# Optimization experiments

Hardware: AMD Instinct MI355X
Metric: run time of the kernel (lower is better)

## Reference

```python
import jax, jax.numpy as jnp
import numpy as np

B, T, E, D, A, H, C, K = 32, 1500, 512, 512, 512, 4, 10, 201
SHARPENING = 1.0


def setup_inputs() -> dict:
    key = jax.random.key(0)
    ks = jax.random.split(key, 11)
    def w(k, shape, fan_in):
        return jax.random.normal(k, shape, jnp.float32) / np.sqrt(fan_in).astype(np.float32)
    return {
        "enc_out": jax.random.normal(ks[0], (B, T, E), jnp.float32),
        "x_lens": jax.random.randint(ks[1], (B,), T // 2, T + 1),
        "dec_out": jax.random.normal(ks[2], (B, 1, D), jnp.float32),
        # previous-step attention weights: a valid distribution over T per head
        "aw_step": jax.nn.softmax(jax.random.normal(ks[3], (B, T, H), jnp.float32), axis=1),
        "w_enc": w(ks[4], (H, E, A), E),   # per-head LinearND(enc->att)
        "b_enc": jnp.zeros((H, A), jnp.float32),
        "w_dec": w(ks[5], (H, D, A), D),   # per-head LinearND(dec->att), no bias
        "w_conv": w(ks[6], (H, C, A), C),  # per-head LinearND(conv_ch->att), no bias
        "conv_k": w(ks[7], (H * C, 1, K), K),  # grouped 1D conv kernels (O,I,K), groups=H
        "v": w(ks[8], (H, A), A),          # per-head LinearND(att->1), no bias
        "w_mha": w(ks[9], (H * E, E), H * E),
        "b_mha": jnp.zeros((E,), jnp.float32),
    }


def reference(enc_out, x_lens, dec_out, aw_step, w_enc, b_enc, w_dec, w_conv, conv_k, v, w_mha, b_mha):
    b, t, e = enc_out.shape
    h = aw_step.shape[-1]
    c = w_conv.shape[1]
    k = conv_k.shape[-1]
    # enc_out_a: per-head encoder projection [B,T,H,A]
    enc_a = jnp.einsum('bte,hea->btha', enc_out, w_enc) + b_enc
    # decoder projection, broadcast over time [B,1,H,A]
    dec_a = jnp.einsum('bd,hda->bha', dec_out[:, 0], w_dec)[:, None]
    # location features: grouped 1D conv over previous attention weights
    aw_t = jnp.transpose(aw_step, (0, 2, 1))  # [B,H,T]
    conv = jax.lax.conv_general_dilated(
        aw_t, conv_k, window_strides=(1,), padding=[(k // 2, k // 2)],
        dimension_numbers=('NCH', 'OIH', 'NCH'), feature_group_count=h)  # [B,H*C,T]
    conv = conv.reshape(b, h, c, t).transpose(0, 3, 1, 2)  # [B,T,H,C]
    conv_a = jnp.einsum('bthc,hca->btha', conv, w_conv)
    # additive energy [B,T,H]
    energy = jnp.einsum('btha,ha->bth', jnp.tanh(enc_a + dec_a + conv_a), v)
    # original code multiplies energy by mask (1 valid, -1024 padded) then sharpening
    mask = jnp.where(jnp.arange(t)[None, :] < x_lens[:, None], 1.0, -1024.0).astype(energy.dtype)
    energy = energy * mask[:, :, None] * SHARPENING
    aw = jax.nn.softmax(energy, axis=1)  # softmax over time per head
    # per-head context, concatenated along feature dim -> [B,1,H*E]
    ctx = jnp.einsum('bte,bth->bhe', enc_out, aw).reshape(b, 1, h * e)
    ctx = ctx @ w_mha + b_mha  # [B,1,E]
    return ctx, aw
```

## Files before the change

### kernel.cpp

```cpp
#include <hip/hip_runtime.h>
#include <hip/hip_bf16.h>

#define BB 32
#define TT 1500
#define TP 1536
#define EE 512
#define HH 4
#define AA 512
#define NN 2048
#define CC 10
#define KCONV 201
#define KAUG 576

typedef __attribute__((ext_vector_type(8))) __bf16 bf16x8;
typedef __attribute__((ext_vector_type(4))) float f32x4;

__device__ __forceinline__ unsigned short f2bf(float x) {
    unsigned int u = __float_as_uint(x);
    u = (u + 0x7fffu + ((u >> 16) & 1u)) >> 16;
    return (unsigned short)u;
}
__device__ __forceinline__ float bf2f(unsigned short u) {
    return __uint_as_float(((unsigned int)u) << 16);
}
__device__ __forceinline__ void glds16(const void* g, void* l) {
    __builtin_amdgcn_global_load_lds(
        (const __attribute__((address_space(1))) unsigned int*)g,
        (__attribute__((address_space(3))) unsigned int*)l, 16, 0, 0);
}
__device__ __forceinline__ float tanh_fast(float x) {
    float e = __expf(x * 2.0f);
    return fmaf(-2.0f, __builtin_amdgcn_rcpf(e + 1.0f), 1.0f);
}

#define PREP_DEC0   0
#define PREP_CONV0  1024
#define PREP_WT0    8704
#define PREP_PAD0   13312
#define PREP_ENC0   20404
#define PREP_TOTAL  44404

__global__ __launch_bounds__(256) void k_prep(
    const float* __restrict__ enc, const int* __restrict__ xl,
    const float* __restrict__ dec_out, const float* __restrict__ aw_step,
    const float* __restrict__ w_enc, const float* __restrict__ b_enc,
    const float* __restrict__ w_dec, const float* __restrict__ w_conv,
    const float* __restrict__ conv_k,
    unsigned short* __restrict__ Whi, unsigned short* __restrict__ Wlo,
    unsigned short* __restrict__ Ahi, unsigned short* __restrict__ Alo,
    float* __restrict__ dec_a) {
    __shared__ float sbuf[456 + KCONV];
    const int bid = blockIdx.x;
    const int tid = threadIdx.x;

    if (bid < PREP_CONV0) {
        const int b  = bid >> 5;
        const int n0 = (bid & 31) * 64;
        const int n  = n0 + (tid & 63);
        const int dg = tid >> 6;
        const int h  = n >> 9, a = n & 511;
        const float* dp = dec_out + (size_t)b * 512 + dg * 128;
        const float* wp = w_dec + ((size_t)h * 512 + dg * 128) * 512 + a;
        float acc = 0.f;
#pragma unroll 8
        for (int d = 0; d < 128; ++d) acc += dp[d] * wp[(size_t)d * 512];
        sbuf[tid] = acc;
        __syncthreads();
        if (tid < 64) {
            float tot = sbuf[tid] + sbuf[tid + 64] + sbuf[tid + 128] + sbuf[tid + 192];
            dec_a[(size_t)b * NN + n0 + tid] = b_enc[n0 + tid] + tot;
        }
    } else if (bid < PREP_WT0) {
        int r = bid - PREP_CONV0;
        const int tch = r % 6;
        const int hc  = (r / 6) % 40;
        const int b   = r / 240;
        const int h   = hc / 10;
        const int t0  = tch * 256;
        float* sAw = sbuf;
        float* sK  = sbuf + 456;
        for (int i = tid; i < 456; i += 256) {
            int ts = t0 - 100 + i;
            sAw[i] = (ts >= 0 && ts < TT) ? aw_step[((size_t)b * TT + ts) * HH + h] : 0.f;
        }
        if (tid < KCONV) sK[tid] = conv_k[(size_t)hc * KCONV + tid];
        __syncthreads();
        int t = t0 + tid;
        if (t < TT) {
            float acc = 0.f;
            for (int k = 0; k < KCONV; ++k) acc += sAw[tid + k] * sK[k];
            size_t o = ((size_t)b * TP + t) * KAUG + 512 + hc;
            unsigned short hi = f2bf(acc);
            Ahi[o] = hi; Alo[o] = f2bf(acc - bf2f(hi));
        }
    } else if (bid < PREP_PAD0) {
        int idx = (bid - PREP_WT0) * 256 + tid;
        int n = idx / KAUG, k = idx % KAUG;
        int h = n >> 9, a = n & 511;
        float val = 0.f;
        if (k < 512) {
            val = w_enc[((size_t)h * 512 + k) * 512 + a];
        } else if (k < 552) {
            int j = k - 512; int h2 = j / 10, c = j % 10;
            if (h2 == h) val = w_conv[((size_t)h * 10 + c) * 512 + a];
        }
        unsigned short hi = f2bf(val);
        Whi[idx] = hi;
        Wlo[idx] = f2bf(val - bf2f(hi));
    } else if (bid < PREP_ENC0) {
        int idx = (bid - PREP_PAD0) * 256 + tid;
        const int tot1 = BB * 36 * KAUG;
        const int tot2 = BB * TT * 24;
        size_t o;
        if (idx < tot1) {
            int b = idx / (36 * KAUG); int r2 = idx % (36 * KAUG);
            int t = 1500 + r2 / KAUG;  int k = r2 % KAUG;
            o = ((size_t)b * TP + t) * KAUG + k;
        } else if (idx < tot1 + tot2) {
            int j = idx - tot1;
            int b = j / (TT * 24); int r2 = j % (TT * 24);
            int t = r2 / 24;       int k = 552 + r2 % 24;
            o = ((size_t)b * TP + t) * KAUG + k;
        } else return;
        Ahi[o] = 0; Alo[o] = 0;
    } else {
        long idx = (long)(bid - PREP_ENC0) * 256 + tid;
        if (idx >= 6144000L) return;
        long f = idx * 4;
        int b = (int)(f / 768000);
        int r2 = (int)(f % 768000);
        int t = r2 >> 9, e = r2 & 511;
        float4 vv = *reinterpret_cast<const float4*>(enc + f);
        ushort4 h4;
        h4.x = f2bf(vv.x); h4.y = f2bf(vv.y); h4.z = f2bf(vv.z); h4.w = f2bf(vv.w);
        size_t o = ((size_t)b * TP + t) * KAUG + e;
        *reinterpret_cast<ushort4*>(Ahi + o) = h4;
        if (((t & ~127) + 128) > xl[b]) {
            ushort4 l4;
            l4.x = f2bf(vv.x - bf2f(h4.x));
            l4.y = f2bf(vv.y - bf2f(h4.y));
            l4.z = f2bf(vv.z - bf2f(h4.z));
            l4.w = f2bf(vv.w - bf2f(h4.w));
            *reinterpret_cast<ushort4*>(Alo + o) = l4;
        }
    }
}

__global__ __launch_bounds__(256) void k_gemm(
    const unsigned short* __restrict__ Ahi, const unsigned short* __restrict__ Alo,
    const unsigned short* __restrict__ Whi, const unsigned short* __restrict__ Wlo,
    const float* __restrict__ dec_a, const float* __restrict__ vvec,
    const int* __restrict__ xl, float* __restrict__ energy) {
    __shared__ unsigned short lsAhi[128 * 32], lsAlo[128 * 32];
    __shared__ unsigned short lsBhi[128 * 32], lsBlo[128 * 32];
    const int ntile = blockIdx.x, mtile = blockIdx.y, b = blockIdx.z;
    const int tid = threadIdx.x;
    const int lane = tid & 63, wave = tid >> 6;
    const int wm = wave >> 1, wn = wave & 1;
    const int m0 = mtile * 128, n0 = ntile * 128;
    const int xlen = xl[b];

    f32x4 acc[4][4];
#pragma unroll
    for (int i = 0; i < 4; i++)
#pragma unroll
        for (int j = 0; j < 4; j++) acc[i][j] = (f32x4){0.f, 0.f, 0.f, 0.f};

    const int row = tid >> 2;
    const int ko  = (tid & 3) * 8;
    const size_t abase = ((size_t)b * TP + m0 + row) * KAUG + ko;
    const size_t bbase = ((size_t)n0 + row) * KAUG + ko;
    const int l1 = row * 32 + ko;
    const int l2 = l1 + 64 * 32;
    const int ar = wm * 64, br = wn * 64;
    const int fo = (lane & 15) * 32 + (lane >> 4) * 8;

    if (m0 + 128 > xlen) {
        for (int ks = 0; ks < 18; ++ks) {
            const int k0 = ks * 32;
            __syncthreads();
            glds16(Ahi + abase + k0,                     &lsAhi[l1]);
            glds16(Ahi + abase + k0 + (size_t)64 * KAUG, &lsAhi[l2]);
            glds16(Alo + abase + k0,                     &lsAlo[l1]);
            glds16(Alo + abase + k0 + (size_t)64 * KAUG, &lsAlo[l2]);
            glds16(Whi + bbase + k0,                     &lsBhi[l1]);
            glds16(Whi + bbase + k0 + (size_t)64 * KAUG, &lsBhi[l2]);
            glds16(Wlo + bbase + k0,                     &lsBlo[l1]);
            glds16(Wlo + bbase + k0 + (size_t)64 * KAUG, &lsBlo[l2]);
            asm volatile("s_waitcnt vmcnt(0)" ::: "memory");
            __syncthreads();

            bf16x8 ah[4], al[4], bh[4], bl[4];
#pragma unroll
            for (int i = 0; i < 4; i++) {
                ah[i] = *(const bf16x8*)&lsAhi[(ar + i * 16) * 32 + fo];
                al[i] = *(const bf16x8*)&lsAlo[(ar + i * 16) * 32 + fo];
                bh[i] = *(const bf16x8*)&lsBhi[(br + i * 16) * 32 + fo];
                bl[i] = *(const bf16x8*)&lsBlo[(br + i * 16) * 32 + fo];
            }
#pragma unroll
            for (int i = 0; i < 4; i++)
#pragma unroll
                for (int j = 0; j < 4; j++) {
                    acc[i][j] = __builtin_amdgcn_mfma_f32_16x16x32_bf16(ah[i], bh[j], acc[i][j], 0, 0, 0);
                    acc[i][j] = __builtin_amdgcn_mfma_f32_16x16x32_bf16(ah[i], bl[j], acc[i][j], 0, 0, 0);
                    acc[i][j] = __builtin_amdgcn_mfma_f32_16x16x32_bf16(al[i], bh[j], acc[i][j], 0, 0, 0);
                }
        }
    } else {
        for (int ks = 0; ks < 18; ++ks) {
            const int k0 = ks * 32;
            __syncthreads();
            glds16(Ahi + abase + k0,                     &lsAhi[l1]);
            glds16(Ahi + abase + k0 + (size_t)64 * KAUG, &lsAhi[l2]);
            glds16(Whi + bbase + k0,                     &lsBhi[l1]);
            glds16(Whi + bbase + k0 + (size_t)64 * KAUG, &lsBhi[l2]);
            asm volatile("s_waitcnt vmcnt(0)" ::: "memory");
            __syncthreads();

            bf16x8 ah[4], bh[4];
#pragma unroll
            for (int i = 0; i < 4; i++) {
                ah[i] = *(const bf16x8*)&lsAhi[(ar + i * 16) * 32 + fo];
                bh[i] = *(const bf16x8*)&lsBhi[(br + i * 16) * 32 + fo];
            }
#pragma unroll
            for (int i = 0; i < 4; i++)
#pragma unroll
                for (int j = 0; j < 4; j++)
                    acc[i][j] = __builtin_amdgcn_mfma_f32_16x16x32_bf16(ah[i], bh[j], acc[i][j], 0, 0, 0);
        }
    }

    const int h = ntile >> 2;
    const int kg = lane >> 4;
    float dv[4], vv[4];
#pragma unroll
    for (int j = 0; j < 4; j++) {
        int ng = n0 + wn * 64 + j * 16 + (lane & 15);
        dv[j] = dec_a[(size_t)b * NN + ng];
        vv[j] = vvec[ng];
    }
#pragma unroll
    for (int i = 0; i < 4; i++) {
        float part[4] = {0.f, 0.f, 0.f, 0.f};
#pragma unroll
        for (int j = 0; j < 4; j++)
#pragma unroll
            for (int r = 0; r < 4; r++)
                part[r] += tanh_fast(acc[i][j][r] + dv[j]) * vv[j];
#pragma unroll
        for (int r = 0; r < 4; r++) {
            float s = part[r];
            s += __shfl_xor(s, 1, 64);
            s += __shfl_xor(s, 2, 64);
            s += __shfl_xor(s, 4, 64);
            s += __shfl_xor(s, 8, 64);
            if ((lane & 15) == 0) {
                int t = m0 + wm * 64 + i * 16 + kg * 4 + r;
                if (t < TT)
                    atomicAdd(&energy[((size_t)b * HH + h) * TP + t], s);
            }
        }
    }
}

__global__ __launch_bounds__(512) void k_softmax(const float* __restrict__ energy,
                                                 const int* __restrict__ x_lens,
                                                 float* __restrict__ aw) {
    const int b = blockIdx.x >> 2, h = blockIdx.x & 3;
    const int tid = threadIdx.x;
    __shared__ float sE[TT];
    __shared__ float red[512];
    const int xlen = x_lens[b];
    float lmax = -3.4e38f;
    for (int t = tid; t < TT; t += 512) {
        float e = energy[((size_t)b * HH + h) * TP + t];
        float m = (t < xlen) ? e : e * -1024.0f;
        sE[t] = m;
        lmax = fmaxf(lmax, m);
    }
    red[tid] = lmax; __syncthreads();
    for (int s = 256; s > 0; s >>= 1) { if (tid < s) red[tid] = fmaxf(red[tid], red[tid + s]); __syncthreads(); }
    float mx = red[0]; __syncthreads();
    float lsum = 0.f;
    for (int t = tid; t < TT; t += 512) {
        float ex = expf(sE[t] - mx);
        sE[t] = ex; lsum += ex;
    }
    red[tid] = lsum; __syncthreads();
    for (int s = 256; s > 0; s >>= 1) { if (tid < s) red[tid] += red[tid + s]; __syncthreads(); }
    float sum = red[0];
    for (int t = tid; t < TT; t += 512)
        aw[((size_t)b * TT + t) * HH + h] = sE[t] / sum;
}

__global__ __launch_bounds__(512) void k_ctx(const float* __restrict__ enc,
                                             const float* __restrict__ aw,
                                             float* __restrict__ ctx_h) {
    const int chunk = blockIdx.x, b = blockIdx.y;
    const int t0 = chunk * 128;
    const int nt = (TT - t0 < 128) ? (TT - t0) : 128;
    __shared__ float sA[128 * 4];
    const int tid = threadIdx.x;
    for (int i = tid; i < nt * 4; i += 512)
        sA[i] = aw[((size_t)b * TT + t0) * HH + i];
    __syncthreads();
    float a0 = 0.f, a1 = 0.f, a2 = 0.f, a3 = 0.f;
    const float* ep = enc + ((size_t)b * TT + t0) * EE + tid;
    if (nt == 128) {
#pragma unroll 8
        for (int tt = 0; tt < 128; ++tt) {
            float ev = ep[(size_t)tt * EE];
            a0 += sA[tt * 4 + 0] * ev; a1 += sA[tt * 4 + 1] * ev;
            a2 += sA[tt * 4 + 2] * ev; a3 += sA[tt * 4 + 3] * ev;
        }
    } else {
        for (int tt = 0; tt < nt; ++tt) {
            float ev = ep[(size_t)tt * EE];
            a0 += sA[tt * 4 + 0] * ev; a1 += sA[tt * 4 + 1] * ev;
            a2 += sA[tt * 4 + 2] * ev; a3 += sA[tt * 4 + 3] * ev;
        }
    }
    atomicAdd(&ctx_h[((size_t)b * HH + 0) * EE + tid], a0);
    atomicAdd(&ctx_h[((size_t)b * HH + 1) * EE + tid], a1);
    atomicAdd(&ctx_h[((size_t)b * HH + 2) * EE + tid], a2);
    atomicAdd(&ctx_h[((size_t)b * HH + 3) * EE + tid], a3);
}

__global__ __launch_bounds__(256) void k_mha(const float* __restrict__ ctx_h,
                                             const float* __restrict__ w_mha,
                                             const float* __restrict__ b_mha,
                                             float* __restrict__ out) {
    __shared__ float sred[256];
    const int tid = threadIdx.x;
    const int b  = blockIdx.x >> 2;
    const int eo = ((blockIdx.x & 3) << 7) + (tid & 127);
    const int kg = tid >> 7;
    const float* c = ctx_h + (size_t)b * NN + kg * 1024;
    const float* w = w_mha + ((size_t)kg * 1024) * EE + eo;
    float acc = 0.f;
#pragma unroll 8
    for (int k = 0; k < 1024; ++k) acc += c[k] * w[(size_t)k * EE];
    sred[tid] = acc;
    __syncthreads();
    if (tid < 128)
        out[(size_t)b * EE + eo] = b_mha[eo] + sred[tid] + sred[tid + 128];
}

extern "C" void kernel_launch(void* const* d_in, const int* in_sizes, int n_in,
                              void* d_out, int out_size, void* d_ws, size_t ws_size,
                              hipStream_t stream) {
    (void)in_sizes; (void)n_in; (void)out_size;
    const float* enc    = (const float*)d_in[0];
    const int*   xlen   = (const int*)d_in[1];
    const float* dec    = (const float*)d_in[2];
    const float* aw_in  = (const float*)d_in[3];
    const float* w_enc  = (const float*)d_in[4];
    const float* b_enc  = (const float*)d_in[5];
    const float* w_dec  = (const float*)d_in[6];
    const float* w_conv = (const float*)d_in[7];
    const float* convk  = (const float*)d_in[8];
    const float* v      = (const float*)d_in[9];
    const float* w_mha  = (const float*)d_in[10];
    const float* b_mha  = (const float*)d_in[11];
    float* out = (float*)d_out;

    char* ws = (char*)d_ws;
    unsigned short* Whi = (unsigned short*)ws;
    unsigned short* Wlo = Whi + (size_t)NN * KAUG;
    unsigned short* Ahi = (unsigned short*)(ws + 4718592);
    unsigned short* Alo = Ahi + (size_t)BB * TP * KAUG;
    float* dec_a  = (float*)(ws + 117964800);
    float* energy = (float*)(ws + 118226944);
    float* ctx_h  = (float*)(ws + 119013376);
    (void)ws_size;

    hipMemsetAsync(energy, 0, 786432 + 262144, stream);

    k_prep<<<dim3(PREP_TOTAL), 256, 0, stream>>>(enc, xlen, dec, aw_in, w_enc, b_enc,
                                                 w_dec, w_conv, convk,
                                                 Whi, Wlo, Ahi, Alo, dec_a);
    k_gemm<<<dim3(16, 12, BB), 256, 0, stream>>>(Ahi, Alo, Whi, Wlo, dec_a, v, xlen, energy);
    k_softmax<<<dim3(BB * HH), 512, 0, stream>>>(energy, xlen, out + 16384);
    k_ctx <<<dim3(12, BB), 512, 0, stream>>>(enc, out + 16384, ctx_h);
    k_mha <<<dim3(128), 256, 0, stream>>>(ctx_h, w_mha, b_mha, out);
}
```

Baseline: 597.1 us.

## Fuse fp32-to-bf16 encoder conversion into GEMM for fully valid tiles

After: 603.9 us. About the same (+1.1%).

```diff
diff --git a/kernel.cpp b/kernel.cpp
--- a/kernel.cpp
+++ b/kernel.cpp
@@ -32,13 +32,18 @@
     float e = __expf(x * 2.0f);
     return fmaf(-2.0f, __builtin_amdgcn_rcpf(e + 1.0f), 1.0f);
 }
+__device__ __forceinline__ unsigned int pkbf(float x, float y) {
+    float2 f{x, y};
+    __hip_bfloat162 h2 = __float22bfloat162_rn(f);
+    return *reinterpret_cast<unsigned int*>(&h2);
+}
 
 #define PREP_DEC0   0
 #define PREP_CONV0  1024
 #define PREP_WT0    8704
 #define PREP_PAD0   13312
 #define PREP_ENC0   20404
-#define PREP_TOTAL  44404
+#define PREP_TOTAL  34740
 
 __global__ __launch_bounds__(256) void k_prep(
     const float* __restrict__ enc, const int* __restrict__ xl,
@@ -91,7 +96,8 @@
             for (int k = 0; k < KCONV; ++k) acc += sAw[tid + k] * sK[k];
             size_t o = ((size_t)b * TP + t) * KAUG + 512 + hc;
             unsigned short hi = f2bf(acc);
-            Ahi[o] = hi; Alo[o] = f2bf(acc - bf2f(hi));
+            Ahi[o] = hi;
+            if (((t & ~127) + 128) > xl[b]) Alo[o] = f2bf(acc - bf2f(hi));
         }
     } else if (bid < PREP_PAD0) {
         int idx = (bid - PREP_WT0) * 256 + tid;
@@ -124,41 +130,40 @@
         } else return;
         Ahi[o] = 0; Alo[o] = 0;
     } else {
-        long idx = (long)(bid - PREP_ENC0) * 256 + tid;
-        if (idx >= 6144000L) return;
-        long f = idx * 4;
-        int b = (int)(f / 768000);
-        int r2 = (int)(f % 768000);
-        int t = r2 >> 9, e = r2 & 511;
-        float4 vv = *reinterpret_cast<const float4*>(enc + f);
-        ushort4 h4;
-        h4.x = f2bf(vv.x); h4.y = f2bf(vv.y); h4.z = f2bf(vv.z); h4.w = f2bf(vv.w);
-        size_t o = ((size_t)b * TP + t) * KAUG + e;
+        int r = bid - PREP_ENC0;
+        int b = r / 448;
+        int f4 = (r % 448) * 256 + tid;
+        int rowoff = f4 >> 7;
+        int col = (f4 & 127) * 4;
+        int rstart = xl[b] & ~127;
+        int t = rstart + rowoff;
+        if (t >= TT) return;
+        float4 vv = *reinterpret_cast<const float4*>(enc + ((size_t)b * TT + t) * 512 + col);
+        ushort4 h4, l4;
+        h4.x = f2bf(vv.x); l4.x = f2bf(vv.x - bf2f(h4.x));
+        h4.y = f2bf(vv.y); l4.y = f2bf(vv.y - bf2f(h4.y));
+        h4.z = f2bf(vv.z); l4.z = f2bf(vv.z - bf2f(h4.z));
+        h4.w = f2bf(vv.w); l4.w = f2bf(vv.w - bf2f(h4.w));
+        size_t o = ((size_t)b * TP + t) * KAUG + col;
         *reinterpret_cast<ushort4*>(Ahi + o) = h4;
-        if (((t & ~127) + 128) > xl[b]) {
-            ushort4 l4;
-            l4.x = f2bf(vv.x - bf2f(h4.x));
-            l4.y = f2bf(vv.y - bf2f(h4.y));
-            l4.z = f2bf(vv.z - bf2f(h4.z));
-            l4.w = f2bf(vv.w - bf2f(h4.w));
-            *reinterpret_cast<ushort4*>(Alo + o) = l4;
-        }
-    }
-}
-
-__global__ __launch_bounds__(256) void k_gemm(
-    const unsigned short* __restrict__ Ahi, const unsigned short* __restrict__ Alo,
-    const unsigned short* __restrict__ Whi, const unsigned short* __restrict__ Wlo,
+        *reinterpret_cast<ushort4*>(Alo + o) = l4;
+    }
+}
+
+__global__ __launch_bounds__(256) void k_gemm_v(
+    const float* __restrict__ enc,
+    const unsigned short* __restrict__ Ahi,
+    const unsigned short* __restrict__ Whi,
     const float* __restrict__ dec_a, const float* __restrict__ vvec,
     const int* __restrict__ xl, float* __restrict__ energy) {
-    __shared__ unsigned short lsAhi[128 * 32], lsAlo[128 * 32];
-    __shared__ unsigned short lsBhi[128 * 32], lsBlo[128 * 32];
+    __shared__ unsigned short lsA[128 * 32];
+    __shared__ unsigned short lsB[128 * 32];
     const int ntile = blockIdx.x, mtile = blockIdx.y, b = blockIdx.z;
+    const int m0 = mtile * 128, n0 = ntile * 128;
+    if (m0 + 128 > xl[b]) return;
     const int tid = threadIdx.x;
     const int lane = tid & 63, wave = tid >> 6;
     const int wm = wave >> 1, wn = wave & 1;
-    const int m0 = mtile * 128, n0 = ntile * 128;
-    const int xlen = xl[b];
 
     f32x4 acc[4][4];
 #pragma unroll
@@ -168,68 +173,60 @@
 
     const int row = tid >> 2;
     const int ko  = (tid & 3) * 8;
+    const size_t bbase = ((size_t)n0 + row) * KAUG + ko;
     const size_t abase = ((size_t)b * TP + m0 + row) * KAUG + ko;
-    const size_t bbase = ((size_t)n0 + row) * KAUG + ko;
-    const int l1 = row * 32 + ko;
+    const int l1 = tid * 8;
     const int l2 = l1 + 64 * 32;
+
+    const float* ap0 = enc + ((size_t)b * TT + m0 + row) * 512 + ko;
+    const float* ap1 = ap0 + (size_t)64 * 512;
+
     const int ar = wm * 64, br = wn * 64;
     const int fo = (lane & 15) * 32 + (lane >> 4) * 8;
 
-    if (m0 + 128 > xlen) {
-        for (int ks = 0; ks < 18; ++ks) {
-            const int k0 = ks * 32;
-            __syncthreads();
-            glds16(Ahi + abase + k0,                     &lsAhi[l1]);
-            glds16(Ahi + abase + k0 + (size_t)64 * KAUG, &lsAhi[l2]);
-            glds16(Alo + abase + k0,                     &lsAlo[l1]);
-            glds16(Alo + abase + k0 + (size_t)64 * KAUG, &lsAlo[l2]);
-            glds16(Whi + bbase + k0,                     &lsBhi[l1]);
-            glds16(Whi + bbase + k0 + (size_t)64 * KAUG, &lsBhi[l2]);
-            glds16(Wlo + bbase + k0,                     &lsBlo[l1]);
-            glds16(Wlo + bbase + k0 + (size_t)64 * KAUG, &lsBlo[l2]);
-            asm volatile("s_waitcnt vmcnt(0)" ::: "memory");
-            __syncthreads();
-
-            bf16x8 ah[4], al[4], bh[4], bl[4];
-#pragma unroll
-            for (int i = 0; i < 4; i++) {
-                ah[i] = *(const bf16x8*)&lsAhi[(ar + i * 16) * 32 + fo];
-                al[i] = *(const bf16x8*)&lsAlo[(ar + i * 16) * 32 + fo];
-                bh[i] = *(const bf16x8*)&lsBhi[(br + i * 16) * 32 + fo];
-                bl[i] = *(const bf16x8*)&lsBlo[(br + i * 16) * 32 + fo];
+    float4 fa0 = *(const float4*)(ap0);
+    float4 fa1 = *(const float4*)(ap0 + 4);
+    float4 fa2 = *(const float4*)(ap1);
+    float4 fa3 = *(const float4*)(ap1 + 4);
+
+    for (int ks = 0; ks < 18; ++ks) {
+        const int k0 = ks * 32;
+        __syncthreads();
+        glds16(Whi + bbase + k0,                     &lsB[l1]);
+        glds16(Whi + bbase + k0 + (size_t)64 * KAUG, &lsB[l2]);
+        if (ks < 16) {
+            uint4 w0, w1;
+            w0.x = pkbf(fa0.x, fa0.y); w0.y = pkbf(fa0.z, fa0.w);
+            w0.z = pkbf(fa1.x, fa1.y); w0.w = pkbf(fa1.z, fa1.w);
+            w1.x = pkbf(fa2.x, fa2.y); w1.y = pkbf(fa2.z, fa2.w);
+            w1.z = pkbf(fa3.x, fa3.y); w1.w = pkbf(fa3.z, fa3.w);
+            *reinterpret_cast<uint4*>(&lsA[l1]) = w0;
+            *reinterpret_cast<uint4*>(&lsA[l1 + 2048]) = w1;
+            if (ks < 15) {
+                const int nk = k0 + 32;
+                fa0 = *(const float4*)(ap0 + nk);
+                fa1 = *(const float4*)(ap0 + nk + 4);
+                fa2 = *(const float4*)(ap1 + nk);
+                fa3 = *(const float4*)(ap1 + nk + 4);
             }
-#pragma unroll
-            for (int i = 0; i < 4; i++)
-#pragma unroll
-                for (int j = 0; j < 4; j++) {
-                    acc[i][j] = __builtin_amdgcn_mfma_f32_16x16x32_bf16(ah[i], bh[j], acc[i][j], 0, 0, 0);
-                    acc[i][j] = __builtin_amdgcn_mfma_f32_16x16x32_bf16(ah[i], bl[j], acc[i][j], 0, 0, 0);
-                    acc[i][j] = __builtin_amdgcn_mfma_f32_16x16x32_bf16(al[i], bh[j], acc[i][j], 0, 0, 0);
-                }
-        }
-    } else {
-        for (int ks = 0; ks < 18; ++ks) {
-            const int k0 = ks * 32;
-            __syncthreads();
-            glds16(Ahi + abase + k0,                     &lsAhi[l1]);
-            glds16(Ahi + abase + k0 + (size_t)64 * KAUG, &lsAhi[l2]);
-            glds16(Whi + bbase + k0,                     &lsBhi[l1]);
-            glds16(Whi + bbase + k0 + (size_t)64 * KAUG, &lsBhi[l2]);
-            asm volatile("s_waitcnt vmcnt(0)" ::: "memory");
-            __syncthreads();
-
-            bf16x8 ah[4], bh[4];
-#pragma unroll
-            for (int i = 0; i < 4; i++) {
-                ah[i] = *(const bf16x8*)&lsAhi[(ar + i * 16) * 32 + fo];
-                bh[i] = *(const bf16x8*)&lsBhi[(br + i * 16) * 32 + fo];
-            }
-#pragma unroll
-            for (int i = 0; i < 4; i++)
-#pragma unroll
-                for (int j = 0; j < 4; j++)
-                    acc[i][j] = __builtin_amdgcn_mfma_f32_16x16x32_bf16(ah[i], bh[j], acc[i][j], 0, 0, 0);
-        }
+        } else {
+            glds16(Ahi + abase + k0,                     &lsA[l1]);
+            glds16(Ahi + abase + k0 + (size_t)64 * KAUG, &lsA[l2]);
+        }
+        asm volatile("s_waitcnt vmcnt(0)" ::: "memory");
+        __syncthreads();
+
+        bf16x8 ah[4], bh[4];
+#pragma unroll
+        for (int i = 0; i < 4; i++) {
+            ah[i] = *(const bf16x8*)&lsA[(ar + i * 16) * 32 + fo];
+            bh[i] = *(const bf16x8*)&lsB[(br + i * 16) * 32 + fo];
+        }
+#pragma unroll
+        for (int i = 0; i < 4; i++)
+#pragma unroll
+            for (int j = 0; j < 4; j++)
+                acc[i][j] = __builtin_amdgcn_mfma_f32_16x16x32_bf16(ah[i], bh[j], acc[i][j], 0, 0, 0);
     }
 
     const int h = ntile >> 2;
@@ -265,34 +262,129 @@
     }
 }
 
-__global__ __launch_bounds__(512) void k_softmax(const float* __restrict__ energy,
-                                                 const int* __restrict__ x_lens,
-                                                 float* __restrict__ aw) {
+__global__ __launch_bounds__(256) void k_gemm_p(
+    const unsigned short* __restrict__ Ahi, const unsigned short* __restrict__ Alo,
+    const unsigned short* __restrict__ Whi, const unsigned short* __restrict__ Wlo,
+    const float* __restrict__ dec_a, const float* __restrict__ vvec,
+    const int* __restrict__ xl, float* __restrict__ energy) {
+    __shared__ unsigned short lsAhi[128 * 32], lsAlo[128 * 32];
+    __shared__ unsigned short lsBhi[128 * 32], lsBlo[128 * 32];
+    const int ntile = blockIdx.x, mtile = blockIdx.y, b = blockIdx.z;
+    const int m0 = mtile * 128, n0 = ntile * 128;
+    if (m0 + 128 <= xl[b]) return;
+    const int tid = threadIdx.x;
+    const int lane = tid & 63, wave = tid >> 6;
+    const int wm = wave >> 1, wn = wave & 1;
+
+    f32x4 acc[4][4];
+#pragma unroll
+    for (int i = 0; i < 4; i++)
+#pragma unroll
+        for (int j = 0; j < 4; j++) acc[i][j] = (f32x4){0.f, 0.f, 0.f, 0.f};
+
+    const int row = tid >> 2;
+    const int ko  = (tid & 3) * 8;
+    const size_t abase = ((size_t)b * TP + m0 + row) * KAUG + ko;
+    const size_t bbase = ((size_t)n0 + row) * KAUG + ko;
+    const int l1 = tid * 8;
+    const int l2 = l1 + 64 * 32;
+    const int ar = wm * 64, br = wn * 64;
+    const int fo = (lane & 15) * 32 + (lane >> 4) * 8;
+
+    for (int ks = 0; ks < 18; ++ks) {
+        const int k0 = ks * 32;
+        __syncthreads();
+        glds16(Ahi + abase + k0,                     &lsAhi[l1]);
+        glds16(Ahi + abase + k0 + (size_t)64 * KAUG, &lsAhi[l2]);
+        glds16(Alo + abase + k0,                     &lsAlo[l1]);
+        glds16(Alo + abase + k0 + (size_t)64 * KAUG, &lsAlo[l2]);
+        glds16(Whi + bbase + k0,                     &lsBhi[l1]);
+        glds16(Whi + bbase + k0 + (size_t)64 * KAUG, &lsBhi[l2]);
+        glds16(Wlo + bbase + k0,                     &lsBlo[l1]);
+        glds16(Wlo + bbase + k0 + (size_t)64 * KAUG, &lsBlo[l2]);
+        asm volatile("s_waitcnt vmcnt(0)" ::: "memory");
+        __syncthreads();
+
+        bf16x8 ah[4], al[4], bh[4], bl[4];
+#pragma unroll
+        for (int i = 0; i < 4; i++) {
+            ah[i] = *(const bf16x8*)&lsAhi[(ar + i * 16) * 32 + fo];
+            al[i] = *(const bf16x8*)&lsAlo[(ar + i * 16) * 32 + fo];
+            bh[i] = *(const bf16x8*)&lsBhi[(br + i * 16) * 32 + fo];
+            bl[i] = *(const bf16x8*)&lsBlo[(br + i * 16) * 32 + fo];
+        }
+#pragma unroll
+        for (int i = 0; i < 4; i++)
+#pragma unroll
+            for (int j = 0; j < 4; j++) {
+                acc[i][j] = __builtin_amdgcn_mfma_f32_16x16x32_bf16(ah[i], bh[j], acc[i][j], 0, 0, 0);
+                acc[i][j] = __builtin_amdgcn_mfma_f32_16x16x32_bf16(ah[i], bl[j], acc[i][j], 0, 0, 0);
+                acc[i][j] = __builtin_amdgcn_mfma_f32_16x16x32_bf16(al[i], bh[j], acc[i][j], 0, 0, 0);
+            }
+    }
+
+    const int h = ntile >> 2;
+    const int kg = lane >> 4;
+    float dv[4], vv[4];
+#pragma unroll
+    for (int j = 0; j < 4; j++) {
+        int ng = n0 + wn * 64 + j * 16 + (lane & 15);
+        dv[j] = dec_a[(size_t)b * NN + ng];
+        vv[j] = vvec[ng];
+    }
+#pragma unroll
+    for (int i = 0; i < 4; i++) {
+        float part[4] = {0.f, 0.f, 0.f, 0.f};
+#pragma unroll
+        for (int j = 0; j < 4; j++)
+#pragma unroll
+            for (int r = 0; r < 4; r++)
+                part[r] += tanh_fast(acc[i][j][r] + dv[j]) * vv[j];
+#pragma unroll
+        for (int r = 0; r < 4; r++) {
+            float s = part[r];
+            s += __shfl_xor(s, 1, 64);
+            s += __shfl_xor(s, 2, 64);
+            s += __shfl_xor(s, 4, 64);
+            s += __shfl_xor(s, 8, 64);
+            if ((lane & 15) == 0) {
+                int t = m0 + wm * 64 + i * 16 + kg * 4 + r;
+                if (t < TT)
+                    atomicAdd(&energy[((size_t)b * HH + h) * TP + t], s);
+            }
+        }
+    }
+}
+
+__global__ __launch_bounds__(1024) void k_softmax(const float* __restrict__ energy,
+                                                  const int* __restrict__ x_lens,
+                                                  float* __restrict__ aw) {
     const int b = blockIdx.x >> 2, h = blockIdx.x & 3;
     const int tid = threadIdx.x;
     __shared__ float sE[TT];
-    __shared__ float red[512];
+    __shared__ float red[1024];
     const int xlen = x_lens[b];
     float lmax = -3.4e38f;
-    for (int t = tid; t < TT; t += 512) {
+    for (int t = tid; t < TT; t += 1024) {
         float e = energy[((size_t)b * HH + h) * TP + t];
         float m = (t < xlen) ? e : e * -1024.0f;
         sE[t] = m;
         lmax = fmaxf(lmax, m);
     }
     red[tid] = lmax; __syncthreads();
-    for (int s = 256; s > 0; s >>= 1) { if (tid < s) red[tid] = fmaxf(red[tid], red[tid + s]); __syncthreads(); }
+    for (int s = 512; s > 0; s >>= 1) { if (tid < s) red[tid] = fmaxf(red[tid], red[tid + s]); __syncthreads(); }
     float mx = red[0]; __syncthreads();
     float lsum = 0.f;
-    for (int t = tid; t < TT; t += 512) {
-        float ex = expf(sE[t] - mx);
+    for (int t = tid; t < TT; t += 1024) {
+        float ex = __expf((sE[t] - mx) * 1.44269504088896341f);
         sE[t] = ex; lsum += ex;
     }
     red[tid] = lsum; __syncthreads();
-    for (int s = 256; s > 0; s >>= 1) { if (tid < s) red[tid] += red[tid + s]; __syncthreads(); }
+    for (int s = 512; s > 0; s >>= 1) { if (tid < s) red[tid] += red[tid + s]; __syncthreads(); }
     float sum = red[0];
-    for (int t = tid; t < TT; t += 512)
-        aw[((size_t)b * TT + t) * HH + h] = sE[t] / sum;
+    float rs = 1.0f / sum;
+    for (int t = tid; t < TT; t += 1024)
+        aw[((size_t)b * TT + t) * HH + h] = sE[t] * rs;
 }
 
 __global__ __launch_bounds__(512) void k_ctx(const float* __restrict__ enc,
@@ -381,8 +473,9 @@
     k_prep<<<dim3(PREP_TOTAL), 256, 0, stream>>>(enc, xlen, dec, aw_in, w_enc, b_enc,
                                                  w_dec, w_conv, convk,
                                                  Whi, Wlo, Ahi, Alo, dec_a);
-    k_gemm<<<dim3(16, 12, BB), 256, 0, stream>>>(Ahi, Alo, Whi, Wlo, dec_a, v, xlen, energy);
-    k_softmax<<<dim3(BB * HH), 512, 0, stream>>>(energy, xlen, out + 16384);
+    k_gemm_v<<<dim3(16, 12, BB), 256, 0, stream>>>(enc, Ahi, Whi, dec_a, v, xlen, energy);
+    k_gemm_p<<<dim3(16, 12, BB), 256, 0, stream>>>(Ahi, Alo, Whi, Wlo, dec_a, v, xlen, energy);
+    k_softmax<<<dim3(BB * HH), 1024, 0, stream>>>(energy, xlen, out + 16384);
     k_ctx <<<dim3(12, BB), 512, 0, stream>>>(enc, out + 16384, ctx_h);
     k_mha <<<dim3(128), 256, 0, stream>>>(ctx_h, w_mha, b_mha, out);
 }
```
